# Kernel optimization log

Measured on AMD Instinct MI355X. Metric: run time of the kernel, lower is better.

Reference implementation:

```python
import jax, jax.numpy as jnp
import numpy as np
import math


def _rel_pos_tables(W):
    # continuous relative coords table: [(2W-1), (2W-1), 2]
    c = np.arange(-(W - 1), W, dtype=np.float32)
    table = np.stack(np.meshgrid(c, c, indexing='ij'), axis=-1)  # [2W-1,2W-1,2]
    table = table / (W - 1)
    table = table * 8.0
    table = np.sign(table) * np.log2(np.abs(table) + 1.0) / math.log2(8.0)
    # relative position index: [W*W, W*W]
    coords = np.stack(np.meshgrid(np.arange(W), np.arange(W), indexing='ij'))  # [2,W,W]
    flat = coords.reshape(2, -1)  # [2, W*W]
    rel = flat[:, :, None] - flat[:, None, :]  # [2, N, N]
    rel = rel.transpose(1, 2, 0).copy()
    rel[:, :, 0] += W - 1
    rel[:, :, 1] += W - 1
    rel[:, :, 0] *= 2 * W - 1
    idx = rel.sum(-1)  # [N, N]
    return jnp.asarray(table), jnp.asarray(idx, dtype=jnp.int32)


def setup_inputs() -> dict:
    key = jax.random.key(0)
    ks = jax.random.split(key, 10)
    dim, W, H = 512, 8, 16
    N = W * W
    B_, nW = 2048, 256
    s = 0.02
    inp = {
        'x': jax.random.normal(ks[0], (B_, N, dim), jnp.float32),
        'mask': jax.random.normal(ks[1], (nW, N, N), jnp.float32),
        'qkv_w': jax.random.normal(ks[2], (dim, 3 * dim), jnp.float32) * s,
        'qkv_b': jnp.zeros((3 * dim,), jnp.float32),
        'logit_scale': jnp.full((H, 1, 1), math.log(10.0), jnp.float32),
        'cpb_w1': jax.random.normal(ks[3], (2, 512), jnp.float32) * s,
        'cpb_b1': jnp.zeros((512,), jnp.float32),
        'cpb_w2': jax.random.normal(ks[4], (512, H), jnp.float32) * s,
        'proj_w': jax.random.normal(ks[5], (dim, dim), jnp.float32) * s,
        'proj_b': jnp.zeros((dim,), jnp.float32),
        'window_size': W,
        'num_heads': H,
    }
    return inp


def reference(x, mask, qkv_w, qkv_b, logit_scale, cpb_w1, cpb_b1, cpb_w2,
              proj_w, proj_b, window_size, num_heads):
    B_, N, C = x.shape
    H = num_heads
    hd = C // H

    qkv = (x @ qkv_w + qkv_b).reshape(B_, N, 3, H, hd)
    qkv = jnp.transpose(qkv, (2, 0, 3, 1, 4))  # [3, B_, H, N, hd]
    q, k, v = qkv[0], qkv[1], qkv[2]

    # cosine attention: L2-normalize q, k (eps matches F.normalize)
    q = q / jnp.clip(jnp.linalg.norm(q, axis=-1, keepdims=True), 1e-12)
    k = k / jnp.clip(jnp.linalg.norm(k, axis=-1, keepdims=True), 1e-12)

    attn = jnp.einsum('bhnd,bhmd->bhnm', q, k)
    scale = jnp.exp(jnp.minimum(logit_scale, math.log(1.0 / 0.01)))  # [H,1,1]
    attn = attn * scale[None]

    # continuous relative position bias
    table, idx = _rel_pos_tables(window_size)
    t = jax.nn.relu(table @ cpb_w1 + cpb_b1) @ cpb_w2  # [2W-1, 2W-1, H]
    t = t.reshape(-1, H)
    bias = t[idx.reshape(-1)].reshape(N, N, H)
    bias = 16.0 * jax.nn.sigmoid(jnp.transpose(bias, (2, 0, 1)))  # [H, N, N]
    attn = attn + bias[None]

    # mask add: [nW, N, N]
    nW = mask.shape[0]
    attn = attn.reshape(B_ // nW, nW, H, N, N) + mask[None, :, None]
    attn = attn.reshape(B_, H, N, N)

    attn = jax.nn.softmax(attn, axis=-1)
    out = jnp.einsum('bhnm,bhmd->bhnd', attn, v)
    out = jnp.transpose(out, (0, 2, 1, 3)).reshape(B_, N, C)
    out = out @ proj_w + proj_b
    return out
```

## Files before the change

kernel.cpp:

```cpp
#include <hip/hip_runtime.h>
#include <hip/hip_bf16.h>
#include <stdint.h>

typedef __attribute__((ext_vector_type(8))) short short8;
typedef __attribute__((ext_vector_type(8))) _Float16 half8;
typedef __attribute__((ext_vector_type(4))) float f32x4;

#define HSTR ((size_t)131072 * 32)

__device__ __forceinline__ unsigned short f2h(float f) {
  union { _Float16 h; unsigned short u; } c;
  c.h = (_Float16)f;
  return c.u;
}
__device__ __forceinline__ float h2f(unsigned short u) {
  union { _Float16 h; unsigned short u; } c;
  c.u = u;
  return (float)c.h;
}
__device__ __forceinline__ void gload_lds16(const void* g, void* l) {
  __builtin_amdgcn_global_load_lds(
      (const __attribute__((address_space(1))) unsigned int*)g,
      (__attribute__((address_space(3))) unsigned int*)l, 16, 0, 0);
}


__global__ __launch_bounds__(256) void cast_f16(const float* __restrict__ in,
                                                unsigned short* __restrict__ out) {
  const size_t total = (size_t)131072 * 512 / 8;
  size_t stride = (size_t)gridDim.x * 256;
  for (size_t i = blockIdx.x * 256 + threadIdx.x; i < total; i += stride) {
    f32x4 f0 = *(const f32x4*)(in + i * 8);
    f32x4 f1 = *(const f32x4*)(in + i * 8 + 4);
    short8 o;
#pragma unroll
    for (int e = 0; e < 4; e++) {
      o[e] = (short)f2h(f0[e]);
      o[4 + e] = (short)f2h(f1[e]);
    }
    *(short8*)(out + i * 8) = o;
  }
}

__global__ __launch_bounds__(256) void transpose_cast(const float* __restrict__ in,
                                                      unsigned short* __restrict__ out,
                                                      int K, int N) {
  __shared__ float tile[32][33];
  int nb = N / 32;
  int bx = blockIdx.x % nb, by = blockIdx.x / nb;
  int tx = threadIdx.x & 31, ty = threadIdx.x >> 5;
#pragma unroll
  for (int r = 0; r < 32; r += 8)
    tile[ty + r][tx] = in[(size_t)(by * 32 + ty + r) * N + bx * 32 + tx];
  __syncthreads();
#pragma unroll
  for (int r = 0; r < 32; r += 8)
    out[(size_t)(bx * 32 + ty + r) * K + by * 32 + tx] = f2h(tile[tx][ty + r]);
}

__device__ __forceinline__ float cpb_coord(int a) {
  float v = (float)(a - 7) * (8.0f / 7.0f);
  float s = (v > 0.f) ? 1.f : ((v < 0.f) ? -1.f : 0.f);
  return s * log2f(fabsf(v) + 1.f) * (1.f / 3.f);
}

__global__ __launch_bounds__(64) void cpb_mlp(const float* __restrict__ w1,
                                              const float* __restrict__ b1,
                                              const float* __restrict__ w2,
                                              float* __restrict__ t_out) {
  int e = blockIdx.x;
  int dy = e / 15, dx = e % 15;
  float in0 = cpb_coord(dy), in1 = cpb_coord(dx);
  float acc[16];
#pragma unroll
  for (int o = 0; o < 16; ++o) acc[o] = 0.f;
  for (int u = threadIdx.x; u < 512; u += 64) {
    float hsum = fmaxf(in0 * w1[u] + in1 * w1[512 + u] + b1[u], 0.f);
#pragma unroll
    for (int o = 0; o < 16; ++o) acc[o] += hsum * w2[u * 16 + o];
  }
#pragma unroll
  for (int o = 0; o < 16; ++o) {
    float v = acc[o];
    v += __shfl_xor(v, 1);  v += __shfl_xor(v, 2);  v += __shfl_xor(v, 4);
    v += __shfl_xor(v, 8);  v += __shfl_xor(v, 16); v += __shfl_xor(v, 32);
    acc[o] = v;
  }
  if (threadIdx.x == 0)
#pragma unroll
    for (int o = 0; o < 16; ++o) t_out[e * 16 + o] = acc[o];
}

__global__ __launch_bounds__(256) void bias_kernel(const float* __restrict__ t,
                                                   float* __restrict__ bias) {
  int idx = blockIdx.x * 256 + threadIdx.x;
  int j = idx & 63, i = (idx >> 6) & 63, h = idx >> 12;
  int dy = (i >> 3) - (j >> 3) + 7;
  int dx = (i & 7) - (j & 7) + 7;
  float v = t[(dy * 15 + dx) * 16 + h];
  bias[idx] = 16.f / (1.f + expf(-v));
}

__global__ __launch_bounds__(512, 1) void qkv_gemm(const unsigned short* __restrict__ xh,
                                                   const unsigned short* __restrict__ Wt,
                                                   const float* __restrict__ bvec,
                                                   unsigned short* __restrict__ qout,
                                                   unsigned short* __restrict__ kout,
                                                   unsigned short* __restrict__ vout) {
  __shared__ __align__(16) short smem[49152];
  const int bid = (blockIdx.x & 7) * 384 + (blockIdx.x >> 3);
  const int nt = bid % 6;
  const int mt = bid / 6;
  const int m0 = mt * 256, n0 = nt * 256;
  const int t = threadIdx.x;
  const int l = t & 63, wid = t >> 6;
  const int wm = wid >> 2, wn = wid & 3;
  const int fr = l & 15, fg = l >> 4;

  f32x4 acc[8][4];
#pragma unroll
  for (int i = 0; i < 8; i++)
#pragma unroll
    for (int j = 0; j < 4; j++) acc[i][j] = f32x4{0.f, 0.f, 0.f, 0.f};

  auto STAGE = [&](int bsel, int kt) {
#pragma unroll
    for (int it = 0; it < 2; ++it) {
      int flat = it * 512 + t;
      int row = flat >> 2, s = flat & 3;
      int g = s ^ (row & 3);
      gload_lds16(xh + (size_t)(m0 + row) * 512 + kt * 32 + g * 8,
                  &smem[bsel * 8192 + flat * 8]);
      gload_lds16(Wt + (size_t)(n0 + row) * 512 + kt * 32 + g * 8,
                  &smem[24576 + bsel * 8192 + flat * 8]);
    }
  };

  STAGE(0, 0);
  STAGE(1, 1);
  __builtin_amdgcn_sched_barrier(0);

  for (int kt = 0; kt < 16; ++kt) {
    const int cur = kt % 3;
    if (kt < 14) STAGE((kt + 2) % 3, kt + 2);
    __builtin_amdgcn_sched_barrier(0);
    if (kt < 14)       asm volatile("s_waitcnt vmcnt(8)" ::: "memory");
    else if (kt == 14) asm volatile("s_waitcnt vmcnt(4)" ::: "memory");
    else               asm volatile("s_waitcnt vmcnt(0)" ::: "memory");
    __builtin_amdgcn_sched_barrier(0);
    __builtin_amdgcn_s_barrier();
    __builtin_amdgcn_sched_barrier(0);
    {
      const short* Ab = &smem[cur * 8192];
      const short* Bb = &smem[24576 + cur * 8192];
      half8 bfr[4];
#pragma unroll
      for (int j = 0; j < 4; ++j) {
        int row = wn * 64 + j * 16 + fr;
        bfr[j] = *(const half8*)&Bb[row * 32 + ((fg ^ (row & 3)) << 3)];
      }
#pragma unroll
      for (int i = 0; i < 8; ++i) {
        int rowA = wm * 128 + i * 16 + fr;
        half8 a0 = *(const half8*)&Ab[rowA * 32 + ((fg ^ (rowA & 3)) << 3)];
#pragma unroll
        for (int j = 0; j < 4; ++j)
          acc[i][j] = __builtin_amdgcn_mfma_f32_16x16x32_f16(a0, bfr[j], acc[i][j], 0, 0, 0);
      }
    }
    __builtin_amdgcn_sched_barrier(0);
    __builtin_amdgcn_s_barrier();
    __builtin_amdgcn_sched_barrier(0);
  }

  unsigned short* dst;
  int g0;
  if (nt < 2)      { dst = qout; g0 = nt * 8; }
  else if (nt < 4) { dst = kout; g0 = (nt - 2) * 8; }
  else             { dst = vout; g0 = (nt - 4) * 8; }
#pragma unroll
  for (int hh = 0; hh < 2; ++hh) {
    if (hh) __syncthreads();
    if (wm == hh) {
#pragma unroll
      for (int i = 0; i < 8; ++i)
#pragma unroll
        for (int j = 0; j < 4; ++j) {
          int col = wn * 64 + j * 16 + fr;
          float bb = bvec[n0 + col];
#pragma unroll
          for (int r = 0; r < 4; ++r)
            smem[(i * 16 + fg * 4 + r) * 256 + col] = (short)f2h(acc[i][j][r] + bb);
        }
    }
    __syncthreads();
#pragma unroll
    for (int it = 0; it < 8; ++it) {
      int flat = it * 512 + t;
      int row = flat >> 5, c32 = flat & 31;
      *(short8*)(dst + (size_t)(g0 + (c32 >> 2)) * HSTR +
                 (size_t)(m0 + hh * 128 + row) * 32 + (c32 & 3) * 8) =
          *(short8*)&smem[row * 256 + c32 * 8];
    }
  }
}

__global__ __launch_bounds__(256) void attn_kernel(const unsigned short* __restrict__ qws,
                                                   const unsigned short* __restrict__ kws,
                                                   const unsigned short* __restrict__ vws,
                                                   const float* __restrict__ bias,
                                                   const float* __restrict__ mask,
                                                   const float* __restrict__ logit_scale,
                                                   unsigned short* __restrict__ aout) {
  const int blk = (blockIdx.x & 7) * 4096 + (blockIdx.x >> 3);
  const int h = blk >> 11;
  const int b = blk & 2047;
  const int wmi = b & 255;
  const int t = threadIdx.x, l = t & 63, w = t >> 6;

  __shared__ __align__(16) short qs[64 * 32], ks[64 * 32];
  __shared__ __align__(16) short vt[32 * 72];
  __shared__ __align__(16) short plds[4 * 16 * 72];
  __shared__ float invs[64];

  const float scale = __expf(fminf(logit_scale[h], 4.6051702f));

  {
    const int r = t >> 2, c4 = t & 3;
    const size_t base = (size_t)h * HSTR + (size_t)(b * 64 + r) * 32 + c4 * 8;
    {
      uint4 raw = *(const uint4*)(qws + base);
      unsigned int rr[4] = {raw.x, raw.y, raw.z, raw.w};
      float f[8];
#pragma unroll
      for (int e = 0; e < 4; e++) {
        f[2 * e]     = h2f((unsigned short)(rr[e] & 0xffff));
        f[2 * e + 1] = h2f((unsigned short)(rr[e] >> 16));
      }
      float ss = 0.f;
#pragma unroll
      for (int e = 0; e < 8; e++) ss += f[e] * f[e];
      ss += __shfl_xor(ss, 1);
      ss += __shfl_xor(ss, 2);
      float inv = 1.f / fmaxf(sqrtf(ss), 1e-12f);
      short8 o;
#pragma unroll
      for (int e = 0; e < 8; e++) o[e] = (short)f2h(f[e] * inv);
      *(short8*)&qs[r * 32 + c4 * 8] = o;
    }
    {
      uint4 raw = *(const uint4*)(kws + base);
      unsigned int rr[4] = {raw.x, raw.y, raw.z, raw.w};
      float f[8];
#pragma unroll
      for (int e = 0; e < 4; e++) {
        f[2 * e]     = h2f((unsigned short)(rr[e] & 0xffff));
        f[2 * e + 1] = h2f((unsigned short)(rr[e] >> 16));
      }
      float ss = 0.f;
#pragma unroll
      for (int e = 0; e < 8; e++) ss += f[e] * f[e];
      ss += __shfl_xor(ss, 1);
      ss += __shfl_xor(ss, 2);
      float inv = 1.f / fmaxf(sqrtf(ss), 1e-12f);
      short8 o;
#pragma unroll
      for (int e = 0; e < 8; e++) o[e] = (short)f2h(f[e] * inv);
      *(short8*)&ks[r * 32 + c4 * 8] = o;
    }
    {
      uint4 raw = *(const uint4*)(vws + base);
      unsigned int rr[4] = {raw.x, raw.y, raw.z, raw.w};
#pragma unroll
      for (int e2 = 0; e2 < 4; e2++) {
        vt[(c4 * 8 + 2 * e2 + 0) * 72 + r] = (short)(rr[e2] & 0xffff);
        vt[(c4 * 8 + 2 * e2 + 1) * 72 + r] = (short)(rr[e2] >> 16);
      }
    }
  }
  __syncthreads();

  const int fr = l & 15, fg = l >> 4;
  half8 bq = *(half8*)&qs[(w * 16 + fr) * 32 + fg * 8];

  f32x4 st[4];
#pragma unroll
  for (int kt = 0; kt < 4; kt++) {
    half8 ak = *(half8*)&ks[(kt * 16 + fr) * 32 + fg * 8];
    st[kt] = __builtin_amdgcn_mfma_f32_16x16x32_f16(ak, bq, f32x4{0.f, 0.f, 0.f, 0.f}, 0, 0, 0);
  }
  const int q = w * 16 + fr;
  const int kbase = fg * 4;
  float sv[16];
  float mx = -1e30f;
#pragma unroll
  for (int kt = 0; kt < 4; kt++) {
    f32x4 b4 = *(const f32x4*)&bias[(size_t)(h * 64 + q) * 64 + kt * 16 + kbase];
    f32x4 m4 = *(const f32x4*)&mask[(size_t)(wmi * 64 + q) * 64 + kt * 16 + kbase];
#pragma unroll
    for (int j = 0; j < 4; j++) {
      float xv = st[kt][j] * scale + b4[j] + m4[j];
      sv[kt * 4 + j] = xv;
      mx = fmaxf(mx, xv);
    }
  }
  mx = fmaxf(mx, __shfl_xor(mx, 16));
  mx = fmaxf(mx, __shfl_xor(mx, 32));
  float sum = 0.f;
#pragma unroll
  for (int i2 = 0; i2 < 16; i2++) {
    float p = __expf(sv[i2] - mx);
    sv[i2] = p;
    sum += p;
  }
  sum += __shfl_xor(sum, 16);
  sum += __shfl_xor(sum, 32);

  short* pl = &plds[w * 16 * 72];
#pragma unroll
  for (int kt = 0; kt < 4; kt++)
#pragma unroll
    for (int j = 0; j < 4; j += 2) {
      unsigned int pack = (unsigned int)f2h(sv[kt * 4 + j]) |
                          ((unsigned int)f2h(sv[kt * 4 + j + 1]) << 16);
      *(unsigned int*)&pl[fr * 72 + kt * 16 + kbase + j] = pack;
    }
  if (fg == 0) invs[q] = 1.f / sum;
  __syncthreads();

  half8 pa0 = *(half8*)&pl[fr * 72 + fg * 8];
  half8 pa1 = *(half8*)&pl[fr * 72 + 32 + fg * 8];
#pragma unroll
  for (int nt2 = 0; nt2 < 2; nt2++) {
    half8 bv0 = *(half8*)&vt[(nt2 * 16 + fr) * 72 + fg * 8];
    half8 bv1 = *(half8*)&vt[(nt2 * 16 + fr) * 72 + 32 + fg * 8];
    f32x4 o = f32x4{0.f, 0.f, 0.f, 0.f};
    o = __builtin_amdgcn_mfma_f32_16x16x32_f16(pa0, bv0, o, 0, 0, 0);
    o = __builtin_amdgcn_mfma_f32_16x16x32_f16(pa1, bv1, o, 0, 0, 0);
    const int qo = w * 16 + fg * 4;
    const int hd = nt2 * 16 + fr;
#pragma unroll
    for (int r2 = 0; r2 < 4; r2++) {
      float vv = o[r2] * invs[qo + r2];
      qs[(qo + r2) * 32 + hd] = (short)f2h(vv);
    }
  }
  __syncthreads();
  {
    const int row = t >> 2, c = t & 3;
    *(short8*)(aout + (size_t)h * HSTR + (size_t)(b * 64 + row) * 32 + c * 8) =
        *(short8*)&qs[row * 32 + c * 8];
  }
}

__global__ __launch_bounds__(256) void proj_gemm(const unsigned short* __restrict__ A,
                                                 const unsigned short* __restrict__ Wt,
                                                 const float* __restrict__ bvec,
                                                 float* __restrict__ out) {
  __shared__ __align__(16) short smem[24576];
  const int bid = (blockIdx.x & 7) * 512 + (blockIdx.x >> 3);
  const int nt = bid & 3;
  const int mt = bid >> 2;
  const int m0 = mt * 128, n0 = nt * 128;
  const int t = threadIdx.x;
  const int l = t & 63, w = t >> 6;
  const int wm = w >> 1, wn = w & 1;
  const int fr = l & 15, fg = l >> 4;

  f32x4 acc[4][4];
#pragma unroll
  for (int i = 0; i < 4; i++)
#pragma unroll
    for (int j = 0; j < 4; j++) acc[i][j] = f32x4{0.f, 0.f, 0.f, 0.f};

  auto STAGE = [&](int bsel, int kt) {
#pragma unroll
    for (int it = 0; it < 2; ++it) {
      int flat = it * 256 + t;
      int row = flat >> 2, s = flat & 3;
      int g = s ^ (row & 3);
      gload_lds16(A + (size_t)kt * HSTR + (size_t)(m0 + row) * 32 + g * 8,
                  &smem[bsel * 4096 + flat * 8]);
      gload_lds16(Wt + (size_t)(n0 + row) * 512 + kt * 32 + g * 8,
                  &smem[12288 + bsel * 4096 + flat * 8]);
    }
  };

  STAGE(0, 0);
  STAGE(1, 1);
  __builtin_amdgcn_sched_barrier(0);

  for (int kt = 0; kt < 16; ++kt) {
    const int cur = kt % 3;
    if (kt < 14) STAGE((kt + 2) % 3, kt + 2);
    __builtin_amdgcn_sched_barrier(0);
    if (kt < 14)       asm volatile("s_waitcnt vmcnt(8)" ::: "memory");
    else if (kt == 14) asm volatile("s_waitcnt vmcnt(4)" ::: "memory");
    else               asm volatile("s_waitcnt vmcnt(0)" ::: "memory");
    __builtin_amdgcn_sched_barrier(0);
    __builtin_amdgcn_s_barrier();
    __builtin_amdgcn_sched_barrier(0);
    {
      const short* Ab = &smem[cur * 4096];
      const short* Bb = &smem[12288 + cur * 4096];
      half8 bfr[4];
#pragma unroll
      for (int j = 0; j < 4; ++j) {
        int row = wn * 64 + j * 16 + fr;
        bfr[j] = *(const half8*)&Bb[row * 32 + ((fg ^ (row & 3)) << 3)];
      }
#pragma unroll
      for (int i = 0; i < 4; ++i) {
        int rowA = wm * 64 + i * 16 + fr;
        half8 a0 = *(const half8*)&Ab[rowA * 32 + ((fg ^ (rowA & 3)) << 3)];
#pragma unroll
        for (int j = 0; j < 4; ++j)
          acc[i][j] = __builtin_amdgcn_mfma_f32_16x16x32_f16(a0, bfr[j], acc[i][j], 0, 0, 0);
      }
    }
    __builtin_amdgcn_sched_barrier(0);
    __builtin_amdgcn_s_barrier();
    __builtin_amdgcn_sched_barrier(0);
  }

  float* bounce = (float*)smem;
#pragma unroll
  for (int half = 0; half < 2; ++half) {
    if (half) __syncthreads();
    if (wm == half) {
#pragma unroll
      for (int j = 0; j < 4; j++) {
        int col = wn * 64 + j * 16 + fr;
        float bb = bvec[n0 + col];
#pragma unroll
        for (int i = 0; i < 4; i++) {
          int row0 = i * 16 + fg * 4;
#pragma unroll
          for (int r = 0; r < 4; r++)
            bounce[(row0 + r) * 128 + col] = acc[i][j][r] + bb;
        }
      }
    }
    __syncthreads();
#pragma unroll
    for (int it = 0; it < 8; ++it) {
      int flat = it * 256 + t;
      int row = flat >> 5, c4 = flat & 31;
      *(f32x4*)(out + (size_t)(m0 + half * 64 + row) * 512 + n0 + c4 * 4) =
          *(f32x4*)&bounce[row * 128 + c4 * 4];
    }
    __syncthreads();
  }
}

extern "C" void kernel_launch(void* const* d_in, const int* in_sizes, int n_in,
                              void* d_out, int out_size, void* d_ws, size_t ws_size,
                              hipStream_t stream) {
  const float* x           = (const float*)d_in[0];
  const float* mask        = (const float*)d_in[1];
  const float* qkv_w       = (const float*)d_in[2];
  const float* qkv_b       = (const float*)d_in[3];
  const float* logit_scale = (const float*)d_in[4];
  const float* cpb_w1      = (const float*)d_in[5];
  const float* cpb_b1      = (const float*)d_in[6];
  const float* cpb_w2      = (const float*)d_in[7];
  const float* proj_w      = (const float*)d_in[8];
  const float* proj_b      = (const float*)d_in[9];
  (void)in_sizes; (void)n_in; (void)out_size; (void)ws_size;

  char* p = (char*)d_ws;
  unsigned short* Wqkv_t  = (unsigned short*)p; p += (size_t)1536 * 512 * 2;
  unsigned short* Wproj_t = (unsigned short*)p; p += (size_t)512 * 512 * 2;
  float* t_cpb            = (float*)p;          p += (size_t)225 * 16 * 4;
  float* biasb            = (float*)p;          p += (size_t)16 * 64 * 64 * 4;
  unsigned short* xh      = (unsigned short*)p; p += (size_t)131072 * 512 * 2;
  unsigned short* qbuf    = (unsigned short*)p; p += (size_t)131072 * 512 * 2;
  unsigned short* kbuf    = (unsigned short*)p; p += (size_t)131072 * 512 * 2;
  unsigned short* vbuf    = (unsigned short*)p; p += (size_t)131072 * 512 * 2;
  unsigned short* abuf    = (unsigned short*)p; p += (size_t)131072 * 512 * 2;

  cast_f16<<<2048, 256, 0, stream>>>(x, xh);
  transpose_cast<<<768, 256, 0, stream>>>(qkv_w, Wqkv_t, 512, 1536);
  transpose_cast<<<256, 256, 0, stream>>>(proj_w, Wproj_t, 512, 512);
  cpb_mlp<<<225, 64, 0, stream>>>(cpb_w1, cpb_b1, cpb_w2, t_cpb);
  bias_kernel<<<256, 256, 0, stream>>>(t_cpb, biasb);
  qkv_gemm<<<3072, 512, 0, stream>>>(xh, Wqkv_t, qkv_b, qbuf, kbuf, vbuf);
  attn_kernel<<<32768, 256, 0, stream>>>(qbuf, kbuf, vbuf, biasb, mask, logit_scale, abuf);
  proj_gemm<<<4096, 256, 0, stream>>>(abuf, Wproj_t, proj_b, (float*)d_out);
}
```

Measured before the change: 714.5 us.

## Fuse fp32-to-fp16 input cast into QKV GEMM A-tile loading

Removes the separate cast kernel and the fp16 copy of x; the QKV GEMM now loads fp32 x rows into registers, converts to fp16 and writes the swizzled A tile to LDS in a software-pipelined double register buffer. The B (weight) tile still uses direct global-to-LDS loads. This saves a full write and re-read of the fp16 activation, but each N-tile block now reads fp32 x (twice the bytes per reuse) and uses more registers and VALU work in the main loop.

```diff
diff --git a/kernel.cpp b/kernel.cpp
--- a/kernel.cpp
+++ b/kernel.cpp
@@ -24,23 +24,6 @@
       (__attribute__((address_space(3))) unsigned int*)l, 16, 0, 0);
 }
 
-
-__global__ __launch_bounds__(256) void cast_f16(const float* __restrict__ in,
-                                                unsigned short* __restrict__ out) {
-  const size_t total = (size_t)131072 * 512 / 8;
-  size_t stride = (size_t)gridDim.x * 256;
-  for (size_t i = blockIdx.x * 256 + threadIdx.x; i < total; i += stride) {
-    f32x4 f0 = *(const f32x4*)(in + i * 8);
-    f32x4 f1 = *(const f32x4*)(in + i * 8 + 4);
-    short8 o;
-#pragma unroll
-    for (int e = 0; e < 4; e++) {
-      o[e] = (short)f2h(f0[e]);
-      o[4 + e] = (short)f2h(f1[e]);
-    }
-    *(short8*)(out + i * 8) = o;
-  }
-}
 
 __global__ __launch_bounds__(256) void transpose_cast(const float* __restrict__ in,
                                                       unsigned short* __restrict__ out,
@@ -101,7 +84,7 @@
   bias[idx] = 16.f / (1.f + expf(-v));
 }
 
-__global__ __launch_bounds__(512, 1) void qkv_gemm(const unsigned short* __restrict__ xh,
+__global__ __launch_bounds__(512, 1) void qkv_gemm(const float* __restrict__ x,
                                                    const unsigned short* __restrict__ Wt,
                                                    const float* __restrict__ bvec,
                                                    unsigned short* __restrict__ qout,
@@ -123,30 +106,68 @@
 #pragma unroll
     for (int j = 0; j < 4; j++) acc[i][j] = f32x4{0.f, 0.f, 0.f, 0.f};
 
-  auto STAGE = [&](int bsel, int kt) {
+  const int arow = t >> 1, as0 = (t & 1) * 2;
+  const int ag0 = as0 ^ (arow & 3), ag1 = (as0 + 1) ^ (arow & 3);
+  const float* arowp = x + (size_t)(m0 + arow) * 512;
+
+  auto ISSUE_A = [&](int kt, f32x4 (&pend)[4]) {
+    const float* base = arowp + kt * 32;
+    pend[0] = *(const f32x4*)(base + ag0 * 8);
+    pend[1] = *(const f32x4*)(base + ag0 * 8 + 4);
+    pend[2] = *(const f32x4*)(base + ag1 * 8);
+    pend[3] = *(const f32x4*)(base + ag1 * 8 + 4);
+  };
+  auto WRITE_A = [&](int bsel, f32x4 (&pend)[4]) {
+    short8 o0, o1;
+#pragma unroll
+    for (int e = 0; e < 4; ++e) {
+      o0[e]     = (short)f2h(pend[0][e]);
+      o0[4 + e] = (short)f2h(pend[1][e]);
+      o1[e]     = (short)f2h(pend[2][e]);
+      o1[4 + e] = (short)f2h(pend[3][e]);
+    }
+    *(short8*)&smem[bsel * 8192 + (arow * 4 + as0) * 8] = o0;
+    *(short8*)&smem[bsel * 8192 + (arow * 4 + as0 + 1) * 8] = o1;
+  };
+  auto ISSUE_B = [&](int bsel, int kt) {
 #pragma unroll
     for (int it = 0; it < 2; ++it) {
       int flat = it * 512 + t;
       int row = flat >> 2, s = flat & 3;
       int g = s ^ (row & 3);
-      gload_lds16(xh + (size_t)(m0 + row) * 512 + kt * 32 + g * 8,
-                  &smem[bsel * 8192 + flat * 8]);
       gload_lds16(Wt + (size_t)(n0 + row) * 512 + kt * 32 + g * 8,
                   &smem[24576 + bsel * 8192 + flat * 8]);
     }
   };
 
-  STAGE(0, 0);
-  STAGE(1, 1);
+  f32x4 pend0[4], pend1[4];
+  ISSUE_A(0, pend0);
+  ISSUE_B(0, 0);
+  ISSUE_A(1, pend1);
+  ISSUE_B(1, 1);
   __builtin_amdgcn_sched_barrier(0);
-
-  for (int kt = 0; kt < 16; ++kt) {
+  asm volatile("s_waitcnt vmcnt(6)" ::: "memory");
+  __builtin_amdgcn_sched_barrier(0);
+  WRITE_A(0, pend0);
+  __builtin_amdgcn_sched_barrier(0);
+  asm volatile("s_waitcnt lgkmcnt(0)" ::: "memory");
+  __builtin_amdgcn_sched_barrier(0);
+  __builtin_amdgcn_s_barrier();
+  __builtin_amdgcn_sched_barrier(0);
+
+  auto ITER = [&](int kt, f32x4 (&cons)[4], f32x4 (&prod)[4]) {
     const int cur = kt % 3;
-    if (kt < 14) STAGE((kt + 2) % 3, kt + 2);
-    __builtin_amdgcn_sched_barrier(0);
-    if (kt < 14)       asm volatile("s_waitcnt vmcnt(8)" ::: "memory");
-    else if (kt == 14) asm volatile("s_waitcnt vmcnt(4)" ::: "memory");
-    else               asm volatile("s_waitcnt vmcnt(0)" ::: "memory");
+    if (kt < 14) {
+      ISSUE_A(kt + 2, prod);
+      ISSUE_B((kt + 2) % 3, kt + 2);
+    }
+    __builtin_amdgcn_sched_barrier(0);
+    if (kt < 14) asm volatile("s_waitcnt vmcnt(6)" ::: "memory");
+    else         asm volatile("s_waitcnt vmcnt(0)" ::: "memory");
+    __builtin_amdgcn_sched_barrier(0);
+    if (kt < 15) WRITE_A((kt + 1) % 3, cons);
+    __builtin_amdgcn_sched_barrier(0);
+    asm volatile("s_waitcnt lgkmcnt(0)" ::: "memory");
     __builtin_amdgcn_sched_barrier(0);
     __builtin_amdgcn_s_barrier();
     __builtin_amdgcn_sched_barrier(0);
@@ -171,6 +192,11 @@
     __builtin_amdgcn_sched_barrier(0);
     __builtin_amdgcn_s_barrier();
     __builtin_amdgcn_sched_barrier(0);
+  };
+
+  for (int k2 = 0; k2 < 8; ++k2) {
+    ITER(2 * k2, pend1, pend0);
+    ITER(2 * k2 + 1, pend0, pend1);
   }
 
   unsigned short* dst;
@@ -473,18 +499,16 @@
   unsigned short* Wproj_t = (unsigned short*)p; p += (size_t)512 * 512 * 2;
   float* t_cpb            = (float*)p;          p += (size_t)225 * 16 * 4;
   float* biasb            = (float*)p;          p += (size_t)16 * 64 * 64 * 4;
-  unsigned short* xh      = (unsigned short*)p; p += (size_t)131072 * 512 * 2;
   unsigned short* qbuf    = (unsigned short*)p; p += (size_t)131072 * 512 * 2;
   unsigned short* kbuf    = (unsigned short*)p; p += (size_t)131072 * 512 * 2;
   unsigned short* vbuf    = (unsigned short*)p; p += (size_t)131072 * 512 * 2;
   unsigned short* abuf    = (unsigned short*)p; p += (size_t)131072 * 512 * 2;
 
-  cast_f16<<<2048, 256, 0, stream>>>(x, xh);
   transpose_cast<<<768, 256, 0, stream>>>(qkv_w, Wqkv_t, 512, 1536);
   transpose_cast<<<256, 256, 0, stream>>>(proj_w, Wproj_t, 512, 512);
   cpb_mlp<<<225, 64, 0, stream>>>(cpb_w1, cpb_b1, cpb_w2, t_cpb);
   bias_kernel<<<256, 256, 0, stream>>>(t_cpb, biasb);
-  qkv_gemm<<<3072, 512, 0, stream>>>(xh, Wqkv_t, qkv_b, qbuf, kbuf, vbuf);
+  qkv_gemm<<<3072, 512, 0, stream>>>(x, Wqkv_t, qkv_b, qbuf, kbuf, vbuf);
   attn_kernel<<<32768, 256, 0, stream>>>(qbuf, kbuf, vbuf, biasb, mask, logit_scale, abuf);
   proj_gemm<<<4096, 256, 0, stream>>>(abuf, Wproj_t, proj_b, (float*)d_out);
 }
```

Result: slower. 768.8 us (+7.6%).
